# Kernel tuning notes

Hardware: AMD Instinct MI355X
Metric: run time of the kernel (lower is better)

Reference implementation:

```python
import jax, jax.numpy as jnp
import numpy as np

VOCAB, EMB, HID, LABELS, SEQ = 30522, 768, 1024, 2, 4096


def setup_inputs() -> dict:
    key = jax.random.key(0)
    ks = jax.random.split(key, 8)
    s = 0.02  # keep gate pre-activations in a sane range
    return {
        "sentence": jax.random.randint(ks[0], (SEQ,), 0, VOCAB),
        "emb": jax.random.normal(ks[1], (VOCAB, EMB), jnp.float32),
        "w_ih": jax.random.normal(ks[2], (4 * HID, EMB), jnp.float32) * s,
        "w_hh": jax.random.normal(ks[3], (4 * HID, HID), jnp.float32) * s,
        "b_ih": jax.random.normal(ks[4], (4 * HID,), jnp.float32) * s,
        "b_hh": jax.random.normal(ks[5], (4 * HID,), jnp.float32) * s,
        "w_out": jax.random.normal(ks[6], (LABELS, HID), jnp.float32) * s,
        "b_out": jax.random.normal(ks[7], (LABELS,), jnp.float32) * s,
    }


def reference(sentence, emb, w_ih, w_hh, b_ih, b_hh, w_out, b_out):
    H = w_hh.shape[1]
    x = emb[sentence]                       # [T, E] frozen embedding lookup
    xg = x @ w_ih.T + (b_ih + b_hh)         # [T, 4H] precompute input-to-gate GEMM

    def cell(carry, xgt):
        h, c = carry
        gates = xgt + w_hh @ h              # [4H]
        i, f, g, o = jnp.split(gates, 4)
        i = jax.nn.sigmoid(i)
        f = jax.nn.sigmoid(f)
        g = jnp.tanh(g)
        o = jax.nn.sigmoid(o)
        c = f * c + i * g
        h = o * jnp.tanh(c)
        return (h, c), None

    h0 = jnp.zeros((H,), x.dtype)
    c0 = jnp.zeros((H,), x.dtype)
    (h_T, _), _ = jax.lax.scan(cell, (h0, c0), xg)
    y = h_T @ w_out.T + b_out               # [label_size]
    return jax.nn.log_softmax(y[None, :], axis=-1)  # [1, label_size]
```

## Files before the change

kernel.cpp:

```cpp
#include <hip/hip_runtime.h>
#include <hip/hip_bf16.h>

#define VOCAB 30522
#define EMB   768
#define HID   1024
#define SEQ   4096
#define NG    4096
#define NWG   128
#define RT    256

static __device__ __forceinline__ unsigned short f32_to_bf16(float f) {
  unsigned u = __float_as_uint(f);
  u = (u + 0x7fffu + ((u >> 16) & 1u)) >> 16;
  return (unsigned short)u;
}

#define BM 64
#define BN 64
#define BK 16

__global__ __launch_bounds__(256) void xg_gemm(
    const int* __restrict__ sent, const float* __restrict__ emb,
    const float* __restrict__ w_ih, const float* __restrict__ b_ih,
    const float* __restrict__ b_hh, __hip_bfloat16* __restrict__ xg) {
  __shared__ float As[BK][BM + 4];
  __shared__ float Bs[BK][BN + 4];
  const int tid = threadIdx.x;
  const int n0 = blockIdx.x * BN;
  const int m0 = blockIdx.y * BM;
  const int tx = tid & 15, ty = tid >> 4;
  const int lr = tid >> 2;
  const int lk = (tid & 3) * 4;

  const int arow = sent[m0 + lr];
  const float* aptr = emb + (size_t)arow * EMB + lk;
  const float* bptr = w_ih + (size_t)(n0 + lr) * EMB + lk;

  float acc[4][4] = {};

  for (int k0 = 0; k0 < EMB; k0 += BK) {
    float4 av = *(const float4*)(aptr + k0);
    float4 bv = *(const float4*)(bptr + k0);
    __syncthreads();
    As[lk + 0][lr] = av.x; As[lk + 1][lr] = av.y;
    As[lk + 2][lr] = av.z; As[lk + 3][lr] = av.w;
    Bs[lk + 0][lr] = bv.x; Bs[lk + 1][lr] = bv.y;
    Bs[lk + 2][lr] = bv.z; Bs[lk + 3][lr] = bv.w;
    __syncthreads();
#pragma unroll
    for (int k = 0; k < BK; ++k) {
      float4 a = *(const float4*)&As[k][ty * 4];
      float4 b = *(const float4*)&Bs[k][tx * 4];
      acc[0][0] = fmaf(a.x, b.x, acc[0][0]); acc[0][1] = fmaf(a.x, b.y, acc[0][1]);
      acc[0][2] = fmaf(a.x, b.z, acc[0][2]); acc[0][3] = fmaf(a.x, b.w, acc[0][3]);
      acc[1][0] = fmaf(a.y, b.x, acc[1][0]); acc[1][1] = fmaf(a.y, b.y, acc[1][1]);
      acc[1][2] = fmaf(a.y, b.z, acc[1][2]); acc[1][3] = fmaf(a.y, b.w, acc[1][3]);
      acc[2][0] = fmaf(a.z, b.x, acc[2][0]); acc[2][1] = fmaf(a.z, b.y, acc[2][1]);
      acc[2][2] = fmaf(a.z, b.z, acc[2][2]); acc[2][3] = fmaf(a.z, b.w, acc[2][3]);
      acc[3][0] = fmaf(a.w, b.x, acc[3][0]); acc[3][1] = fmaf(a.w, b.y, acc[3][1]);
      acc[3][2] = fmaf(a.w, b.z, acc[3][2]); acc[3][3] = fmaf(a.w, b.w, acc[3][3]);
    }
  }

#pragma unroll
  for (int i = 0; i < 4; ++i) {
    int gm = m0 + ty * 4 + i;
#pragma unroll
    for (int j = 0; j < 4; ++j) {
      int gn = n0 + tx * 4 + j;
      float v = acc[i][j] + b_ih[gn] + b_hh[gn];
      xg[(size_t)gm * NG + gn] = __float2bfloat16(v);
    }
  }
}

__global__ __launch_bounds__(RT, 1) void lstm_rec(
    const float* __restrict__ w_hh, const __hip_bfloat16* __restrict__ xg,
    unsigned long long* __restrict__ slots) {
  __shared__ unsigned hl[2][512];

  const int tid  = threadIdx.x;
  const int wg   = blockIdx.x;
  const int lane = tid & 63;
  const int wv   = tid >> 6;
  const int c    = lane;
  const int m    = lane & 1;

  unsigned wp[8][8];
#pragma unroll
  for (int s = 0; s < 8; ++s) {
    const int q = s >> 1, mm = s & 1;
    const int gr = q * HID + wg * 8 + 2 * wv + mm;
    const float* wr = w_hh + (size_t)gr * HID;
#pragma unroll
    for (int k = 0; k < 8; ++k) {
      float2 wv2 = *(const float2*)(wr + 2 * (c + 64 * k));
      wp[s][k] = ((unsigned)f32_to_bf16(wv2.y) << 16) | (unsigned)f32_to_bf16(wv2.x);
    }
  }
#pragma unroll
  for (int s = 0; s < 8; ++s)
#pragma unroll
    for (int k = 0; k < 8; ++k)
      asm volatile("" : "+v"(wp[s][k]));

  float cst = 0.f;

  for (int t = 0; t < SEQ; ++t) {
    float xqv = 0.f;
    if (lane < 8) {
      const int q = lane >> 1;
      xqv = __bfloat162float(
          xg[(size_t)t * NG + q * HID + wg * 8 + 2 * wv + (lane & 1)]);
    }

    if (wv == 0) {
      const unsigned long long want = (unsigned long long)t;
      unsigned long long* sb = slots + ((t & 1) << 9);
      unsigned long long v[8];
      for (;;) {
#pragma unroll
        for (int k = 0; k < 8; ++k)
          v[k] = __hip_atomic_load(sb + 64 * k + lane,
                                   __ATOMIC_RELAXED, __HIP_MEMORY_SCOPE_AGENT);
        bool ok = true;
#pragma unroll
        for (int k = 0; k < 8; ++k) ok &= ((v[k] >> 32) == want);
        if (ok) break;
      }
#pragma unroll
      for (int k = 0; k < 8; ++k)
        hl[t & 1][64 * k + lane] = (unsigned)v[k];
    }
    __syncthreads();

    const unsigned* hb = hl[t & 1];
    float hx[8], hy[8];
#pragma unroll
    for (int k = 0; k < 8; ++k) {
      unsigned hw = hb[c + 64 * k];
      hx[k] = __uint_as_float(hw << 16);
      hy[k] = __uint_as_float(hw & 0xffff0000u);
    }

    float acc[8];
#pragma unroll
    for (int s = 0; s < 8; ++s) {
      float a = 0.f;
#pragma unroll
      for (int k = 0; k < 8; ++k) {
        unsigned w = wp[s][k];
        a = fmaf(__uint_as_float(w << 16),         hx[k], a);
        a = fmaf(__uint_as_float(w & 0xffff0000u), hy[k], a);
      }
      acc[s] = a;
    }

#pragma unroll
    for (int M = 1, n = 8; M <= 4; M <<= 1, n >>= 1) {
#pragma unroll
      for (int j = 0; j < 4; ++j) {
        if (j < (n >> 1)) {
          float u  = (lane & M) ? acc[2 * j + 1] : acc[2 * j];
          float u2 = (lane & M) ? acc[2 * j]     : acc[2 * j + 1];
          acc[j] = u + __shfl_xor(u2, M, 64);
        }
      }
    }
    float r = acc[0];
    r += __shfl_xor(r, 8, 64);
    r += __shfl_xor(r, 16, 64);
    r += __shfl_xor(r, 32, 64);

    {
      const int s = lane & 7;
      const bool isg = (s >> 1) == 2;
      float z = r + xqv;
      z = isg ? 2.f * z : z;
      float sg = 1.f / (1.f + __expf(-z));
      r = isg ? fmaf(2.f, sg, -1.f) : sg;
    }

    float i_ = __shfl(r, m,     64);
    float f_ = __shfl(r, 2 + m, 64);
    float g_ = __shfl(r, 4 + m, 64);
    float o_ = __shfl(r, 6 + m, 64);

    cst = fmaf(f_, cst, i_ * g_);
    float th = fmaf(2.f, 1.f / (1.f + __expf(-2.f * cst)), -1.f);
    float hn = o_ * th;

    float hn1 = __shfl(hn, 1, 64);
    if (lane == 0) {
      unsigned payload = ((unsigned)f32_to_bf16(hn1) << 16) | (unsigned)f32_to_bf16(hn);
      unsigned long long pv =
          ((unsigned long long)(unsigned)(t + 1) << 32) | (unsigned long long)payload;
      __hip_atomic_store(slots + (((t + 1) & 1) << 9) + (wg * 4 + wv), pv,
                         __ATOMIC_RELAXED, __HIP_MEMORY_SCOPE_AGENT);
    }
  }
}

__global__ __launch_bounds__(256) void head_kernel(
    const unsigned long long* __restrict__ hslots, const float* __restrict__ w_out,
    const float* __restrict__ b_out, float* __restrict__ out) {
  __shared__ float s0[256], s1[256];
  const int tid = threadIdx.x;
  float p0 = 0.f, p1 = 0.f;
  for (int w = tid; w < 512; w += 256) {
    unsigned pw = (unsigned)hslots[w];
    float h0 = __uint_as_float(pw << 16);
    float h1 = __uint_as_float(pw & 0xffff0000u);
    p0 = fmaf(h0, w_out[2 * w], fmaf(h1, w_out[2 * w + 1], p0));
    p1 = fmaf(h0, w_out[HID + 2 * w], fmaf(h1, w_out[HID + 2 * w + 1], p1));
  }
  s0[tid] = p0; s1[tid] = p1;
  __syncthreads();
  for (int off = 128; off; off >>= 1) {
    if (tid < off) { s0[tid] += s0[tid + off]; s1[tid] += s1[tid + off]; }
    __syncthreads();
  }
  if (tid == 0) {
    float y0 = s0[0] + b_out[0], y1 = s1[0] + b_out[1];
    float mx = fmaxf(y0, y1);
    float lse = mx + logf(expf(y0 - mx) + expf(y1 - mx));
    out[0] = y0 - lse;
    out[1] = y1 - lse;
  }
}

extern "C" void kernel_launch(void* const* d_in, const int* in_sizes, int n_in,
                              void* d_out, int out_size, void* d_ws, size_t ws_size,
                              hipStream_t stream) {
  const int*   sent  = (const int*)d_in[0];
  const float* emb   = (const float*)d_in[1];
  const float* w_ih  = (const float*)d_in[2];
  const float* w_hh  = (const float*)d_in[3];
  const float* b_ih  = (const float*)d_in[4];
  const float* b_hh  = (const float*)d_in[5];
  const float* w_out = (const float*)d_in[6];
  const float* b_out = (const float*)d_in[7];
  float* out = (float*)d_out;

  unsigned long long* slots = (unsigned long long*)d_ws;
  __hip_bfloat16* xg = (__hip_bfloat16*)((char*)d_ws + 16384);

  hipMemsetAsync(d_ws, 0, 16384, stream);

  dim3 ggrid(NG / BN, SEQ / BM);
  xg_gemm<<<ggrid, 256, 0, stream>>>(sent, emb, w_ih, b_ih, b_hh, xg);

  lstm_rec<<<NWG, RT, 0, stream>>>(w_hh, xg, slots);

  head_kernel<<<1, 256, 0, stream>>>(slots, w_out, b_out, out);
}
```

Baseline: 7.486 ms.

## Pipeline xg GEMM into recurrence via per-row-block ready flags

The GEMM now writes its output with packed 64-bit atomic stores and bumps a per-row-block completion counter. The recurrence kernel waits on those counters before consuming each 64-step chunk, so it could start before the whole GEMM finishes. Recurrence slots are now zeroed inside the kernel, which shrinks the memset. Both kernels are launched in order on the same stream, so they probably will not actually overlap; the main concrete change is the vectorized epilogue store.

New measurement: 7.499 ms. Within noise of the previous version (+0.2%).

```diff
diff --git a/kernel.cpp b/kernel.cpp
--- a/kernel.cpp
+++ b/kernel.cpp
@@ -22,7 +22,8 @@
 __global__ __launch_bounds__(256) void xg_gemm(
     const int* __restrict__ sent, const float* __restrict__ emb,
     const float* __restrict__ w_ih, const float* __restrict__ b_ih,
-    const float* __restrict__ b_hh, __hip_bfloat16* __restrict__ xg) {
+    const float* __restrict__ b_hh, unsigned long long* __restrict__ xg64,
+    int* __restrict__ flags) {
   __shared__ float As[BK][BM + 4];
   __shared__ float Bs[BK][BN + 4];
   const int tid = threadIdx.x;
@@ -62,21 +63,31 @@
     }
   }
 
+  const int gbase = n0 + tx * 4;
+  const float b0 = b_ih[gbase]     + b_hh[gbase];
+  const float b1 = b_ih[gbase + 1] + b_hh[gbase + 1];
+  const float b2 = b_ih[gbase + 2] + b_hh[gbase + 2];
+  const float b3 = b_ih[gbase + 3] + b_hh[gbase + 3];
 #pragma unroll
   for (int i = 0; i < 4; ++i) {
-    int gm = m0 + ty * 4 + i;
-#pragma unroll
-    for (int j = 0; j < 4; ++j) {
-      int gn = n0 + tx * 4 + j;
-      float v = acc[i][j] + b_ih[gn] + b_hh[gn];
-      xg[(size_t)gm * NG + gn] = __float2bfloat16(v);
-    }
-  }
+    const int gm = m0 + ty * 4 + i;
+    unsigned lo = ((unsigned)f32_to_bf16(acc[i][1] + b1) << 16) |
+                  (unsigned)f32_to_bf16(acc[i][0] + b0);
+    unsigned hi = ((unsigned)f32_to_bf16(acc[i][3] + b3) << 16) |
+                  (unsigned)f32_to_bf16(acc[i][2] + b2);
+    unsigned long long wrd = ((unsigned long long)hi << 32) | lo;
+    __hip_atomic_store(xg64 + (size_t)gm * (NG / 4) + (gbase >> 2), wrd,
+                       __ATOMIC_RELAXED, __HIP_MEMORY_SCOPE_AGENT);
+  }
+  __syncthreads();
+  if (tid == 0)
+    __hip_atomic_fetch_add(flags + blockIdx.y, 1,
+                           __ATOMIC_RELAXED, __HIP_MEMORY_SCOPE_AGENT);
 }
 
 __global__ __launch_bounds__(RT, 1) void lstm_rec(
-    const float* __restrict__ w_hh, const __hip_bfloat16* __restrict__ xg,
-    unsigned long long* __restrict__ slots) {
+    const float* __restrict__ w_hh, const unsigned* __restrict__ xg32,
+    unsigned long long* __restrict__ slots, int* __restrict__ flags) {
   __shared__ unsigned hl[2][512];
 
   const int tid  = threadIdx.x;
@@ -104,17 +115,32 @@
     for (int k = 0; k < 8; ++k)
       asm volatile("" : "+v"(wp[s][k]));
 
+  if (lane == 0)
+    __hip_atomic_store(slots + (wg * 4 + wv), 0ULL,
+                       __ATOMIC_RELAXED, __HIP_MEMORY_SCOPE_AGENT);
+  if (wv == 0) {
+    while (__hip_atomic_load(flags, __ATOMIC_RELAXED, __HIP_MEMORY_SCOPE_AGENT) < 64) {}
+  }
+  __syncthreads();
+
   float cst = 0.f;
 
   for (int t = 0; t < SEQ; ++t) {
     float xqv = 0.f;
     if (lane < 8) {
       const int q = lane >> 1;
-      xqv = __bfloat162float(
-          xg[(size_t)t * NG + q * HID + wg * 8 + 2 * wv + (lane & 1)]);
+      unsigned w = __hip_atomic_load(
+          xg32 + ((size_t)t * (NG / 2) + q * (HID / 2) + wg * 4 + wv),
+          __ATOMIC_RELAXED, __HIP_MEMORY_SCOPE_AGENT);
+      xqv = __uint_as_float((lane & 1) ? (w & 0xffff0000u) : (w << 16));
     }
 
     if (wv == 0) {
+      if (((t + 1) & 63) == 0 && (t + 1) < SEQ) {
+        const int nb = (t + 1) >> 6;
+        while (__hip_atomic_load(flags + nb, __ATOMIC_RELAXED,
+                                 __HIP_MEMORY_SCOPE_AGENT) < 64) {}
+      }
       const unsigned long long want = (unsigned long long)t;
       unsigned long long* sb = slots + ((t & 1) << 9);
       unsigned long long v[8];
@@ -243,14 +269,16 @@
   float* out = (float*)d_out;
 
   unsigned long long* slots = (unsigned long long*)d_ws;
-  __hip_bfloat16* xg = (__hip_bfloat16*)((char*)d_ws + 16384);
-
-  hipMemsetAsync(d_ws, 0, 16384, stream);
+  int* flags = (int*)((char*)d_ws + 8192);
+  void* xg   = (char*)d_ws + 16384;
+
+  hipMemsetAsync(flags, 0, 256, stream);
 
   dim3 ggrid(NG / BN, SEQ / BM);
-  xg_gemm<<<ggrid, 256, 0, stream>>>(sent, emb, w_ih, b_ih, b_hh, xg);
-
-  lstm_rec<<<NWG, RT, 0, stream>>>(w_hh, xg, slots);
+  xg_gemm<<<ggrid, 256, 0, stream>>>(sent, emb, w_ih, b_ih, b_hh,
+                                     (unsigned long long*)xg, flags);
+
+  lstm_rec<<<NWG, RT, 0, stream>>>(w_hh, (const unsigned*)xg, slots, flags);
 
   head_kernel<<<1, 256, 0, stream>>>(slots, w_out, b_out, out);
 }
```
